# Kernel tuning notes

Measured on AMD Instinct MI355X. Metric: run time of the kernel, lower is better.

The kernel has to match this reference:

```python
import jax, jax.numpy as jnp
import numpy as np

VOCAB = 100000
TABLE = 2 * VOCAB - 1  # 199999
EMB = 256
B = 16384
CTX = 10
INIT_RANGE = 0.5 / EMB


def setup_inputs() -> dict:
    key = jax.random.key(0)
    k1, k2, k3, k4, k5 = jax.random.split(key, 5)
    pos_u = jax.random.randint(k1, (B, CTX), 0, TABLE)
    pos_w = jax.random.randint(k2, (B,), 0, TABLE)
    neg_u = jax.random.randint(k3, (B, CTX), 0, TABLE)
    neg_w = jax.random.randint(k4, (B,), 0, TABLE)
    ku, kw = jax.random.split(k5)
    u_weight = jax.random.uniform(ku, (TABLE, EMB), jnp.float32, -INIT_RANGE, INIT_RANGE)
    # original inits w_embeddings to zeros; use small random so grads are non-trivial
    w_weight = jax.random.normal(kw, (TABLE, EMB), jnp.float32) * 0.01
    return {"pos_u": pos_u, "pos_w": pos_w, "neg_u": neg_u, "neg_w": neg_w,
            "u_weight": u_weight, "w_weight": w_weight}


def reference(pos_u, pos_w, neg_u, neg_w, u_weight, w_weight):
    # context embedding sum: [B, CTX, E] -> [B, E]
    pos_u_emb = jnp.sum(u_weight[pos_u], axis=1)
    neg_u_emb = jnp.sum(u_weight[neg_u], axis=1)
    pos_w_emb = w_weight[pos_w]  # [B, E]
    neg_w_emb = w_weight[neg_w]  # [B, E]
    pos_score = jax.nn.log_sigmoid(jnp.sum(pos_u_emb * pos_w_emb, axis=1))
    neg_score = jax.nn.log_sigmoid(-jnp.sum(neg_u_emb * neg_w_emb, axis=1))
    loss = jnp.sum(pos_score) + jnp.sum(neg_score)
    return -loss
```

## Files before the change

kernel.cpp:

```cpp
#include <hip/hip_runtime.h>

#define BATCH 16384
#define CTX 10
#define EMB 256
#define TASKS (BATCH * 2)
#define BLOCKS (TASKS / 4)

__global__ __launch_bounds__(256) void cbow_loss_kernel(
    const int* __restrict__ pos_u, const int* __restrict__ pos_w,
    const int* __restrict__ neg_u, const int* __restrict__ neg_w,
    const float* __restrict__ u_weight, const float* __restrict__ w_weight,
    float* __restrict__ out)
{
    __shared__ float wave_sum[4];

    const int lane = threadIdx.x & 63;
    const int wave = threadIdx.x >> 6;
    const int task = blockIdx.x * 4 + wave;
    const int b    = task >> 1;
    const int neg  = task & 1;

    const int* __restrict__ uidx = neg ? neg_u : pos_u;
    const int* __restrict__ widx = neg ? neg_w : pos_w;

    const float4* __restrict__ U = (const float4*)u_weight;
    const float4* __restrict__ W = (const float4*)w_weight;

    float4 acc = make_float4(0.f, 0.f, 0.f, 0.f);
    const int* __restrict__ rowp = uidx + b * CTX;
#pragma unroll
    for (int c = 0; c < CTX; ++c) {
        const int r = rowp[c];
        const float4 v = U[(size_t)r * 64 + lane];
        acc.x += v.x; acc.y += v.y; acc.z += v.z; acc.w += v.w;
    }

    const int wr = widx[b];
    const float4 wv = W[(size_t)wr * 64 + lane];

    float p = acc.x * wv.x + acc.y * wv.y + acc.z * wv.z + acc.w * wv.w;

#pragma unroll
    for (int m = 32; m >= 1; m >>= 1)
        p += __shfl_xor(p, m, 64);

    const float x = neg ? -p : p;
    const float ls = fminf(x, 0.f) - log1pf(expf(-fabsf(x)));

    if (lane == 0) wave_sum[wave] = -ls;
    __syncthreads();

    if (threadIdx.x == 0) {
        atomicAdd(out, wave_sum[0] + wave_sum[1] + wave_sum[2] + wave_sum[3]);
    }
}

extern "C" void kernel_launch(void* const* d_in, const int* in_sizes, int n_in,
                              void* d_out, int out_size, void* d_ws, size_t ws_size,
                              hipStream_t stream) {
    const int*   pos_u    = (const int*)d_in[0];
    const int*   pos_w    = (const int*)d_in[1];
    const int*   neg_u    = (const int*)d_in[2];
    const int*   neg_w    = (const int*)d_in[3];
    const float* u_weight = (const float*)d_in[4];
    const float* w_weight = (const float*)d_in[5];
    float*       out      = (float*)d_out;

    hipMemsetAsync(out, 0, sizeof(float), stream);

    cbow_loss_kernel<<<BLOCKS, 256, 0, stream>>>(
        pos_u, pos_w, neg_u, neg_w, u_weight, w_weight, out);
}
```

Before: 411.1 us.

## Process four tasks per wave with lane-distributed index loads and shuffles

Each wave now handles four (batch, pos/neg) tasks instead of one. Lanes 0-10 load the context and word indices for each task in a single coalesced load and broadcast them with shuffles, replacing scalar index loads. The grid is four times smaller, which cuts the number of atomics. This trades fewer waves in flight for more independent gathers per wave, which may lower memory-level parallelism if the compiler serializes the per-task loops.

```diff
diff --git a/kernel.cpp b/kernel.cpp
--- a/kernel.cpp
+++ b/kernel.cpp
@@ -4,7 +4,9 @@
 #define CTX 10
 #define EMB 256
 #define TASKS (BATCH * 2)
-#define BLOCKS (TASKS / 4)
+#define T 4
+#define WAVES 4
+#define BLOCKS (TASKS / (T * WAVES))
 
 __global__ __launch_bounds__(256) void cbow_loss_kernel(
     const int* __restrict__ pos_u, const int* __restrict__ pos_w,
@@ -12,46 +14,61 @@
     const float* __restrict__ u_weight, const float* __restrict__ w_weight,
     float* __restrict__ out)
 {
-    __shared__ float wave_sum[4];
+    __shared__ float wave_sum[WAVES];
 
-    const int lane = threadIdx.x & 63;
-    const int wave = threadIdx.x >> 6;
-    const int task = blockIdx.x * 4 + wave;
-    const int b    = task >> 1;
-    const int neg  = task & 1;
-
-    const int* __restrict__ uidx = neg ? neg_u : pos_u;
-    const int* __restrict__ widx = neg ? neg_w : pos_w;
+    const int lane  = threadIdx.x & 63;
+    const int wave  = threadIdx.x >> 6;
+    const int task0 = (blockIdx.x * WAVES + wave) * T;
 
     const float4* __restrict__ U = (const float4*)u_weight;
     const float4* __restrict__ W = (const float4*)w_weight;
 
-    float4 acc = make_float4(0.f, 0.f, 0.f, 0.f);
-    const int* __restrict__ rowp = uidx + b * CTX;
+    int iv[T];
 #pragma unroll
-    for (int c = 0; c < CTX; ++c) {
-        const int r = rowp[c];
-        const float4 v = U[(size_t)r * 64 + lane];
-        acc.x += v.x; acc.y += v.y; acc.z += v.z; acc.w += v.w;
+    for (int t = 0; t < T; ++t) {
+        const int task = task0 + t;
+        const int b    = task >> 1;
+        const int neg  = task & 1;
+        const int* __restrict__ ui = neg ? neg_u : pos_u;
+        const int* __restrict__ wi = neg ? neg_w : pos_w;
+        int v = 0;
+        if (lane <= CTX) v = (lane < CTX) ? ui[b * CTX + lane] : wi[b];
+        iv[t] = v;
     }
 
-    const int wr = widx[b];
-    const float4 wv = W[(size_t)wr * 64 + lane];
+    float lsum = 0.f;
+#pragma unroll
+    for (int t = 0; t < T; ++t) {
+        const int neg = (task0 + t) & 1;
 
-    float p = acc.x * wv.x + acc.y * wv.y + acc.z * wv.z + acc.w * wv.w;
+        const int wr = __shfl(iv[t], CTX, 64);
+        const float4 wv = W[(size_t)wr * 64 + lane];
 
+        float4 acc = make_float4(0.f, 0.f, 0.f, 0.f);
 #pragma unroll
-    for (int m = 32; m >= 1; m >>= 1)
-        p += __shfl_xor(p, m, 64);
+        for (int c = 0; c < CTX; ++c) {
+            const int r = __shfl(iv[t], c, 64);
+            const float4 v = U[(size_t)r * 64 + lane];
+            acc.x += v.x; acc.y += v.y; acc.z += v.z; acc.w += v.w;
+        }
 
-    const float x = neg ? -p : p;
-    const float ls = fminf(x, 0.f) - log1pf(expf(-fabsf(x)));
+        float p = acc.x * wv.x + acc.y * wv.y + acc.z * wv.z + acc.w * wv.w;
+#pragma unroll
+        for (int m = 32; m >= 1; m >>= 1)
+            p += __shfl_xor(p, m, 64);
 
-    if (lane == 0) wave_sum[wave] = -ls;
+        const float x = neg ? -p : p;
+        lsum += fminf(x, 0.f) - log1pf(expf(-fabsf(x)));
+    }
+
+    if (lane == 0) wave_sum[wave] = -lsum;
     __syncthreads();
 
     if (threadIdx.x == 0) {
-        atomicAdd(out, wave_sum[0] + wave_sum[1] + wave_sum[2] + wave_sum[3]);
+        float s = 0.f;
+#pragma unroll
+        for (int w = 0; w < WAVES; ++w) s += wave_sum[w];
+        atomicAdd(out, s);
     }
 }
 
```

New measurement: 375.2 us. 1.1x faster.
